# Performance work log

Measured on AMD Instinct MI355X. Metric: run time of the kernel, lower is better.

Reference implementation:

```python
import jax, jax.numpy as jnp
import numpy as np

B, S, DIM, H = 4, 4096, 2048, 16
HD = DIM // H  # head_dim = 128


def setup_inputs() -> dict:
    key = jax.random.key(0)
    ks = jax.random.split(key, 6)
    X = jax.random.normal(ks[0], (B, S, DIM), dtype=jnp.float32)
    freqs_cos = jax.random.uniform(ks[1], (S, HD), dtype=jnp.float32)
    freqs_sin = jax.random.uniform(ks[2], (S, HD), dtype=jnp.float32)
    attention_mask = jnp.ones((B, S), dtype=jnp.int32)
    # Linear weights stored as [in, out] (equivalent to torch W.T); no bias.
    scale = 0.02
    Wq = jax.random.normal(ks[3], (DIM, DIM), dtype=jnp.float32) * scale
    Wk = jax.random.normal(ks[4], (DIM, DIM), dtype=jnp.float32) * scale
    Wv = jax.random.normal(ks[5], (DIM, DIM), dtype=jnp.float32) * scale
    return {"X": X, "freqs_cos": freqs_cos, "freqs_sin": freqs_sin,
            "attention_mask": attention_mask, "Wq": Wq, "Wk": Wk, "Wv": Wv}


def _rotate_half_interleaved(x):
    # x: [B, S, H, D]; pairs along last dim: (x0, x1) -> (-x1, x0), interleaved
    xp = x.reshape(*x.shape[:-1], HD // 2, 2)
    xt = jnp.stack([-xp[..., 1], xp[..., 0]], axis=-1)
    return xt.reshape(x.shape)


def reference(X, freqs_cos, freqs_sin, attention_mask, Wq, Wk, Wv):
    bs, seq_len, _ = X.shape
    # QKV projections (no bias), fused view to [B, S, H, HD]
    Xq = (X @ Wq).reshape(bs, seq_len, H, HD)
    Xk = (X @ Wk).reshape(bs, seq_len, H, HD)
    Xv = (X @ Wv).reshape(bs, seq_len, H, HD)
    # RoPE: broadcast freqs to (1, S, 1, HD)
    cos = freqs_cos[None, :, None, :]
    sin = freqs_sin[None, :, None, :]
    Xq_out = Xq * cos + _rotate_half_interleaved(Xq) * sin
    Xk_out = Xk * cos + _rotate_half_interleaved(Xk) * sin
    return (Xq_out, Xk_out, Xv)
```

## Files before the change

kernel.cpp:

```cpp
#include <hip/hip_runtime.h>
#include <hip/hip_bf16.h>
#include <stdint.h>

#define B_    4
#define S_    4096
#define DIM_  2048
#define H_    16
#define HD_   128
#define M_    (B_ * S_)
#define K_    DIM_
#define N_    (3 * DIM_)

typedef __attribute__((ext_vector_type(8))) short bf16x8;
typedef __attribute__((ext_vector_type(4))) float f32x4;

__global__ void cvt_x_kernel(const float* __restrict__ X,
                             __hip_bfloat16* __restrict__ Xb) {
    size_t i = ((size_t)blockIdx.x * 256 + threadIdx.x) * 8;
    float4 a = *reinterpret_cast<const float4*>(X + i);
    float4 b = *reinterpret_cast<const float4*>(X + i + 4);
    union { __hip_bfloat16 h[8]; uint4 u; } o;
    o.h[0] = __float2bfloat16(a.x);
    o.h[1] = __float2bfloat16(a.y);
    o.h[2] = __float2bfloat16(a.z);
    o.h[3] = __float2bfloat16(a.w);
    o.h[4] = __float2bfloat16(b.x);
    o.h[5] = __float2bfloat16(b.y);
    o.h[6] = __float2bfloat16(b.z);
    o.h[7] = __float2bfloat16(b.w);
    *reinterpret_cast<uint4*>(Xb + i) = o.u;
}

__global__ void cvt_w_kernel(const float* __restrict__ Wq,
                             const float* __restrict__ Wk,
                             const float* __restrict__ Wv,
                             __hip_bfloat16* __restrict__ Wt) {
    __shared__ float tile[32][33];
    int w = blockIdx.z;
    const float* W = (w == 0) ? Wq : (w == 1) ? Wk : Wv;
    int n0 = blockIdx.x * 32;
    int k0 = blockIdx.y * 32;
    int tx = threadIdx.x, ty = threadIdx.y;
#pragma unroll
    for (int r = 0; r < 4; ++r) {
        int k = k0 + ty + r * 8;
        tile[ty + r * 8][tx] = W[(size_t)k * DIM_ + n0 + tx];
    }
    __syncthreads();
#pragma unroll
    for (int r = 0; r < 4; ++r) {
        int n = n0 + ty + r * 8;
        Wt[(size_t)(w * DIM_ + n) * K_ + k0 + tx] =
            __float2bfloat16(tile[tx][ty + r * 8]);
    }
}

#define BM 256
#define BN 256
#define BK 64
#define NT (K_ / BK)
#define NU (NT / 2)

#define BAR()      asm volatile("s_barrier" ::: "memory")
#define LGKM8()    asm volatile("s_waitcnt lgkmcnt(8)" ::: "memory")
#define WAIT_VM(n) asm volatile("s_waitcnt vmcnt(" #n ")" ::: "memory")

__global__ __launch_bounds__(512, 1) void gemm_rope_kernel(
    const __hip_bfloat16* __restrict__ Xb,
    const __hip_bfloat16* __restrict__ Wt,
    const float* __restrict__ fcos,
    const float* __restrict__ fsin,
    float* __restrict__ out)
{
    __shared__ __hip_bfloat16 As[2][BM * BK];
    __shared__ __hip_bfloat16 Bs[2][BN * BK];

    int bid   = blockIdx.x;
    int x     = bid & 7;
    int local = bid >> 3;
    int tn = x * 3 + local % 3;
    int tm = local / 3;
    int m0 = tm * BM, n0 = tn * BN;

    int tid  = threadIdx.x;
    int lane = tid & 63;
    int w    = tid >> 6;
    int wr   = w >> 2;
    int wc   = w & 3;

    int rl   = lane >> 3;
    int gsw  = ((lane & 7) ^ rl) * 8;
    int lcol = (lane & 7) * 8;

    int fr = lane & 15;
    int fq = lane >> 4;
    int l7 = lane & 7;
    int ce0 = ((0 + fq) ^ l7) * 8;
    int ce1 = ((4 + fq) ^ l7) * 8;

#define STAGE_A(t, bb, r) do {                                                 \
        const __hip_bfloat16* _s = Xb + (size_t)(m0 + (r) * 64 + w * 8 + rl) * K_ \
                                      + (t) * BK + gsw;                        \
        __hip_bfloat16* _d = &As[bb][((r) * 64 + w * 8 + rl) * BK + lcol];     \
        __builtin_amdgcn_global_load_lds(                                      \
            (const __attribute__((address_space(1))) void*)_s,                 \
            (__attribute__((address_space(3))) void*)_d, 16, 0, 0);            \
    } while (0)

#define STAGE_B(t, bb, r) do {                                                 \
        const __hip_bfloat16* _s = Wt + (size_t)(n0 + (r) * 64 + w * 8 + rl) * K_ \
                                      + (t) * BK + gsw;                        \
        __hip_bfloat16* _d = &Bs[bb][((r) * 64 + w * 8 + rl) * BK + lcol];     \
        __builtin_amdgcn_global_load_lds(                                      \
            (const __attribute__((address_space(1))) void*)_s,                 \
            (__attribute__((address_space(3))) void*)_d, 16, 0, 0);            \
    } while (0)

    f32x4  acc[2][2][4][2] = {};
    bf16x8 a[4][2];
    bf16x8 b[2][2][2];

#define LDA(bb, qi) do {                                                       \
        _Pragma("unroll")                                                      \
        for (int i = 0; i < 4; ++i) {                                          \
            int _row = wr * 128 + (qi) * 64 + i * 16 + fr;                     \
            a[i][0] = *reinterpret_cast<const bf16x8*>(&As[bb][_row * BK + ce0]); \
            a[i][1] = *reinterpret_cast<const bf16x8*>(&As[bb][_row * BK + ce1]); \
        }                                                                      \
    } while (0)

#define LDB(bb, qj) do {                                                       \
        _Pragma("unroll")                                                      \
        for (int j = 0; j < 2; ++j) {                                          \
            int _row = wc * 64 + (qj) * 32 + j * 16 + fr;                      \
            b[qj][j][0] = *reinterpret_cast<const bf16x8*>(&Bs[bb][_row * BK + ce0]); \
            b[qj][j][1] = *reinterpret_cast<const bf16x8*>(&Bs[bb][_row * BK + ce1]); \
        }                                                                      \
    } while (0)

#define MFMA_Q(qi, qj) do {                                                    \
        __builtin_amdgcn_s_setprio(1);                                         \
        _Pragma("unroll")                                                      \
        for (int i = 0; i < 4; ++i)                                            \
        _Pragma("unroll")                                                      \
        for (int j = 0; j < 2; ++j) {                                          \
            acc[qi][qj][i][j] = __builtin_amdgcn_mfma_f32_16x16x32_bf16(       \
                a[i][0], b[qj][j][0], acc[qi][qj][i][j], 0, 0, 0);             \
            acc[qi][qj][i][j] = __builtin_amdgcn_mfma_f32_16x16x32_bf16(       \
                a[i][1], b[qj][j][1], acc[qi][qj][i][j], 0, 0, 0);             \
        }                                                                      \
        __builtin_amdgcn_s_setprio(0);                                         \
    } while (0)

#pragma unroll
    for (int r = 0; r < 4; ++r) STAGE_A(0, 0, r);
#pragma unroll
    for (int r = 0; r < 4; ++r) STAGE_B(0, 0, r);
#pragma unroll
    for (int r = 0; r < 4; ++r) STAGE_B(1, 1, r);
    WAIT_VM(4);
    BAR();

    for (int u = 0; u < NU; ++u) {
        int T0 = 2 * u, T1 = 2 * u + 1;
        bool last = (u == NU - 1);
        LDA(0, 0); LDB(0, 0);
        STAGE_A(T1, 1, 0); STAGE_A(T1, 1, 1);
        LGKM8();
        BAR();
        MFMA_Q(0, 0);
        BAR();
        LDB(0, 1);
        STAGE_A(T1, 1, 2); STAGE_A(T1, 1, 3);
        BAR();
        MFMA_Q(0, 1);
        BAR();
        LDA(0, 1);
        if (!last) { STAGE_B(T0 + 2, 0, 0); STAGE_B(T0 + 2, 0, 1); }
        BAR();
        MFMA_Q(1, 0);
        BAR();
        if (!last) { STAGE_A(T0 + 2, 0, 0); STAGE_A(T0 + 2, 0, 1); }
        BAR();
        MFMA_Q(1, 1);
        if (last) { WAIT_VM(0); } else { WAIT_VM(4); }
        BAR();
        LDA(1, 0); LDB(1, 0);
        if (!last) { STAGE_A(T0 + 2, 0, 2); STAGE_A(T0 + 2, 0, 3); }
        LGKM8();
        BAR();
        MFMA_Q(0, 0);
        BAR();
        LDB(1, 1);
        if (!last) { STAGE_B(T0 + 2, 0, 2); STAGE_B(T0 + 2, 0, 3); }
        BAR();
        MFMA_Q(0, 1);
        BAR();
        LDA(1, 1);
        if (!last) { STAGE_B(T1 + 2, 1, 0); STAGE_B(T1 + 2, 1, 1); }
        BAR();
        MFMA_Q(1, 0);
        BAR();
        if (!last) { STAGE_B(T1 + 2, 1, 2); STAGE_B(T1 + 2, 1, 3); }
        BAR();
        MFMA_Q(1, 1);
        if (!last) { WAIT_VM(4); }
        BAR();
    }

#pragma unroll
    for (int qi = 0; qi < 2; ++qi)
#pragma unroll
    for (int i = 0; i < 4; ++i) {
        int mbase = m0 + wr * 128 + qi * 64 + i * 16 + fq * 4;
#pragma unroll
        for (int qj = 0; qj < 2; ++qj)
#pragma unroll
        for (int j = 0; j < 2; ++j) {
            int n = n0 + wc * 64 + qj * 32 + j * 16 + fr;
            int region = n >> 11;
            int cc = n & (DIM_ - 1);
            int d  = cc & (HD_ - 1);
#pragma unroll
            for (int r = 0; r < 4; ++r) {
                int m = mbase + r;
                int s = m & (S_ - 1);
                float g  = acc[qi][qj][i][j][r];
                float gp = __shfl_xor(g, 1, 64);
                float o;
                if (region < 2) {
                    float cv = fcos[s * HD_ + d];
                    float sv = fsin[s * HD_ + d];
                    o = g * cv + ((cc & 1) ? gp * sv : -gp * sv);
                } else {
                    o = g;
                }
                __builtin_nontemporal_store(
                    o, &out[(size_t)region * M_ * DIM_ + (size_t)m * DIM_ + cc]);
            }
        }
    }
#undef STAGE_A
#undef STAGE_B
#undef LDA
#undef LDB
#undef MFMA_Q
}

extern "C" void kernel_launch(void* const* d_in, const int* in_sizes, int n_in,
                              void* d_out, int out_size, void* d_ws, size_t ws_size,
                              hipStream_t stream) {
    const float* X    = (const float*)d_in[0];
    const float* fcos = (const float*)d_in[1];
    const float* fsin = (const float*)d_in[2];
    const float* Wq   = (const float*)d_in[4];
    const float* Wk   = (const float*)d_in[5];
    const float* Wv   = (const float*)d_in[6];
    float* out = (float*)d_out;

    __hip_bfloat16* Xb  = (__hip_bfloat16*)d_ws;
    __hip_bfloat16* Wtp = Xb + (size_t)M_ * K_;

    {
        int threads = 256;
        int blocks = (M_ * K_) / (threads * 8);
        cvt_x_kernel<<<blocks, threads, 0, stream>>>(X, Xb);
    }
    {
        dim3 grid(DIM_ / 32, DIM_ / 32, 3);
        dim3 block(32, 8);
        cvt_w_kernel<<<grid, block, 0, stream>>>(Wq, Wk, Wv, Wtp);
    }
    {
        int blocks = (M_ / BM) * (N_ / BN);
        gemm_rope_kernel<<<blocks, 512, 0, stream>>>(Xb, Wtp, fcos, fsin, out);
    }
}
```

Measured before the change: 531.0 us.

## Restructure GEMM main loop with double-buffered A fragments and fewer barriers

```diff
diff --git a/kernel.cpp b/kernel.cpp
--- a/kernel.cpp
+++ b/kernel.cpp
@@ -62,8 +62,8 @@
 #define NU (NT / 2)
 
 #define BAR()      asm volatile("s_barrier" ::: "memory")
-#define LGKM8()    asm volatile("s_waitcnt lgkmcnt(8)" ::: "memory")
 #define WAIT_VM(n) asm volatile("s_waitcnt vmcnt(" #n ")" ::: "memory")
+#define SCHEDB()   __builtin_amdgcn_sched_barrier(0)
 
 __global__ __launch_bounds__(512, 1) void gemm_rope_kernel(
     const __hip_bfloat16* __restrict__ Xb,
@@ -117,15 +117,16 @@
     } while (0)
 
     f32x4  acc[2][2][4][2] = {};
-    bf16x8 a[4][2];
-    bf16x8 b[2][2][2];
-
-#define LDA(bb, qi) do {                                                       \
+    bf16x8 bA0[4][2];
+    bf16x8 bA1[4][2];
+    bf16x8 bB[2][2][2];
+
+#define LDA_TO(dst, bb, qi) do {                                               \
         _Pragma("unroll")                                                      \
         for (int i = 0; i < 4; ++i) {                                          \
             int _row = wr * 128 + (qi) * 64 + i * 16 + fr;                     \
-            a[i][0] = *reinterpret_cast<const bf16x8*>(&As[bb][_row * BK + ce0]); \
-            a[i][1] = *reinterpret_cast<const bf16x8*>(&As[bb][_row * BK + ce1]); \
+            dst[i][0] = *reinterpret_cast<const bf16x8*>(&As[bb][_row * BK + ce0]); \
+            dst[i][1] = *reinterpret_cast<const bf16x8*>(&As[bb][_row * BK + ce1]); \
         }                                                                      \
     } while (0)
 
@@ -133,79 +134,65 @@
         _Pragma("unroll")                                                      \
         for (int j = 0; j < 2; ++j) {                                          \
             int _row = wc * 64 + (qj) * 32 + j * 16 + fr;                      \
-            b[qj][j][0] = *reinterpret_cast<const bf16x8*>(&Bs[bb][_row * BK + ce0]); \
-            b[qj][j][1] = *reinterpret_cast<const bf16x8*>(&Bs[bb][_row * BK + ce1]); \
-        }                                                                      \
-    } while (0)
-
-#define MFMA_Q(qi, qj) do {                                                    \
+            bB[qj][j][0] = *reinterpret_cast<const bf16x8*>(&Bs[bb][_row * BK + ce0]); \
+            bB[qj][j][1] = *reinterpret_cast<const bf16x8*>(&Bs[bb][_row * BK + ce1]); \
+        }                                                                      \
+    } while (0)
+
+#define MFMA_Q(A, qi, qj) do {                                                 \
         __builtin_amdgcn_s_setprio(1);                                         \
         _Pragma("unroll")                                                      \
         for (int i = 0; i < 4; ++i)                                            \
         _Pragma("unroll")                                                      \
         for (int j = 0; j < 2; ++j) {                                          \
             acc[qi][qj][i][j] = __builtin_amdgcn_mfma_f32_16x16x32_bf16(       \
-                a[i][0], b[qj][j][0], acc[qi][qj][i][j], 0, 0, 0);             \
+                A[i][0], bB[qj][j][0], acc[qi][qj][i][j], 0, 0, 0);            \
             acc[qi][qj][i][j] = __builtin_amdgcn_mfma_f32_16x16x32_bf16(       \
-                a[i][1], b[qj][j][1], acc[qi][qj][i][j], 0, 0, 0);             \
+                A[i][1], bB[qj][j][1], acc[qi][qj][i][j], 0, 0, 0);            \
         }                                                                      \
         __builtin_amdgcn_s_setprio(0);                                         \
-    } while (0)
-
+        SCHEDB();                                                              \
+    } while (0)
+
+#define DO_TILE(tcur, P, Q) do {                                               \
+                                                                       \
+        LDB(P, 0); LDB(P, 1);                                                  \
+        LDA_TO(bA1, P, 1);                                                     \
+        if ((tcur) + 1 < NT) { STAGE_A((tcur) + 1, Q, 1);                      \
+                               STAGE_A((tcur) + 1, Q, 3); }                    \
+        BAR();                                                                 \
+        MFMA_Q(bA0, 0, 0);                                                     \
+        MFMA_Q(bA0, 0, 1);                                                     \
+                       \
+        WAIT_VM(0);                                                            \
+        BAR();                                                                 \
+        MFMA_Q(bA1, 1, 0);                                                     \
+                                                                       \
+        if ((tcur) + 1 < NT) LDA_TO(bA0, Q, 0);                                \
+        if ((tcur) + 2 < NT) {                                                 \
+            STAGE_B((tcur) + 2, P, 0); STAGE_B((tcur) + 2, P, 1);              \
+            STAGE_B((tcur) + 2, P, 2); STAGE_B((tcur) + 2, P, 3);              \
+            STAGE_A((tcur) + 2, P, 0); STAGE_A((tcur) + 2, P, 2);              \
+        }                                                                      \
+        BAR();                                                                 \
+        MFMA_Q(bA1, 1, 1);                                                     \
+    } while (0)
+
+#pragma unroll
+    for (int r = 0; r < 4; ++r) STAGE_B(0, 0, r);
 #pragma unroll
     for (int r = 0; r < 4; ++r) STAGE_A(0, 0, r);
 #pragma unroll
-    for (int r = 0; r < 4; ++r) STAGE_B(0, 0, r);
-#pragma unroll
     for (int r = 0; r < 4; ++r) STAGE_B(1, 1, r);
-    WAIT_VM(4);
+    STAGE_A(1, 1, 0); STAGE_A(1, 1, 2);
+    WAIT_VM(6);
     BAR();
+    LDA_TO(bA0, 0, 0);
 
     for (int u = 0; u < NU; ++u) {
         int T0 = 2 * u, T1 = 2 * u + 1;
-        bool last = (u == NU - 1);
-        LDA(0, 0); LDB(0, 0);
-        STAGE_A(T1, 1, 0); STAGE_A(T1, 1, 1);
-        LGKM8();
-        BAR();
-        MFMA_Q(0, 0);
-        BAR();
-        LDB(0, 1);
-        STAGE_A(T1, 1, 2); STAGE_A(T1, 1, 3);
-        BAR();
-        MFMA_Q(0, 1);
-        BAR();
-        LDA(0, 1);
-        if (!last) { STAGE_B(T0 + 2, 0, 0); STAGE_B(T0 + 2, 0, 1); }
-        BAR();
-        MFMA_Q(1, 0);
-        BAR();
-        if (!last) { STAGE_A(T0 + 2, 0, 0); STAGE_A(T0 + 2, 0, 1); }
-        BAR();
-        MFMA_Q(1, 1);
-        if (last) { WAIT_VM(0); } else { WAIT_VM(4); }
-        BAR();
-        LDA(1, 0); LDB(1, 0);
-        if (!last) { STAGE_A(T0 + 2, 0, 2); STAGE_A(T0 + 2, 0, 3); }
-        LGKM8();
-        BAR();
-        MFMA_Q(0, 0);
-        BAR();
-        LDB(1, 1);
-        if (!last) { STAGE_B(T0 + 2, 0, 2); STAGE_B(T0 + 2, 0, 3); }
-        BAR();
-        MFMA_Q(0, 1);
-        BAR();
-        LDA(1, 1);
-        if (!last) { STAGE_B(T1 + 2, 1, 0); STAGE_B(T1 + 2, 1, 1); }
-        BAR();
-        MFMA_Q(1, 0);
-        BAR();
-        if (!last) { STAGE_B(T1 + 2, 1, 2); STAGE_B(T1 + 2, 1, 3); }
-        BAR();
-        MFMA_Q(1, 1);
-        if (!last) { WAIT_VM(4); }
-        BAR();
+        DO_TILE(T0, 0, 1);
+        DO_TILE(T1, 1, 0);
     }
 
 #pragma unroll
@@ -242,9 +229,10 @@
     }
 #undef STAGE_A
 #undef STAGE_B
-#undef LDA
+#undef LDA_TO
 #undef LDB
 #undef MFMA_Q
+#undef DO_TILE
 }
 
 extern "C" void kernel_launch(void* const* d_in, const int* in_sizes, int n_in,
```

New measurement: 705.9 us. +32.9%, slower.
